# Kernel tuning notes

Measured on AMD Instinct MI355X. Metric: run time of the kernel, lower is better.

The kernel has to match this reference:

```python
import jax, jax.numpy as jnp
import numpy as np

B, S, D = 1, 2048, 4096
H, KVH, HD = 32, 8, 128
GROUPS = H // KVH  # 4
SCALE = HD ** -0.5
NEG = jnp.finfo(jnp.float32).min


def rotate_half(x):
    x1 = x[..., : x.shape[-1] // 2]
    x2 = x[..., x.shape[-1] // 2:]
    return jnp.concatenate((-x2, x1), axis=-1)


def setup_inputs() -> dict:
    key = jax.random.key(0)
    ks = jax.random.split(key, 8)
    return {
        "hidden_states": jax.random.normal(ks[0], (B, S, D), dtype=jnp.float32),
        "cos": jax.random.uniform(ks[1], (B, S, HD), dtype=jnp.float32),
        "sin": jax.random.uniform(ks[2], (B, S, HD), dtype=jnp.float32),
        "attention_mask": jnp.ones((B, S), dtype=bool),
        "wq": jax.random.normal(ks[3], (D, H * HD), dtype=jnp.float32) * 0.02,
        "wk": jax.random.normal(ks[4], (D, KVH * HD), dtype=jnp.float32) * 0.02,
        "wv": jax.random.normal(ks[5], (D, KVH * HD), dtype=jnp.float32) * 0.02,
        "wo": jax.random.normal(ks[6], (H * HD, D), dtype=jnp.float32) * 0.02,
    }


def reference(hidden_states, cos, sin, attention_mask, wq, wk, wv, wo):
    b, s, _ = hidden_states.shape
    # projections -> (B,S,heads,head_dim)
    q = (hidden_states @ wq).reshape(b, s, H, HD)
    k = (hidden_states @ wk).reshape(b, s, KVH, HD)
    v = (hidden_states @ wv).reshape(b, s, KVH, HD)
    # RoPE (cos/sin unsqueezed at head axis)
    c = cos[:, :, None, :]
    si = sin[:, :, None, :]
    q = q * c + rotate_half(q) * si
    k = k * c + rotate_half(k) * si
    # GQA: repeat kv heads (cache_index=0, max_len==S -> cache write is identity)
    k = jnp.repeat(k, GROUPS, axis=2)
    v = jnp.repeat(v, GROUPS, axis=2)
    # mask: causal AND padding; bias 0 / -inf
    causal = jnp.tril(jnp.ones((s, s), dtype=bool))[None, None]  # (1,1,S,S)
    mask = causal & attention_mask[:, None, None, :]  # (B,1,S,S)
    bias = jnp.where(mask, 0.0, NEG).astype(hidden_states.dtype)
    # scores (B,H,S,S)
    scores = jnp.einsum("bqhd,bkhd->bhqk", q, k) * SCALE + bias
    attn = jax.nn.softmax(scores, axis=-1)
    out = jnp.einsum("bhqk,bkhd->bqhd", attn, v).reshape(b, s, H * HD)
    return out @ wo
```

## Files before the change

### kernel.cpp

```cpp
#include <hip/hip_runtime.h>
#include <hip/hip_bf16.h>

#define SEQ   2048
#define DM    4096
#define NH    32
#define NKVH  8
#define HD    128
#define NQKV  6144
#define KOFF  4096
#define VOFF  5120
#define QLD   5120
#define SCALE 0.08838834764831845f

typedef __attribute__((ext_vector_type(4))) float f32x4;
typedef __attribute__((ext_vector_type(8))) short short8;

__device__ __forceinline__ unsigned short f2bf(float f) {
  union { float f; unsigned int u; } v; v.f = f;
  unsigned int r = v.u + 0x7FFF + ((v.u >> 16) & 1);
  return (unsigned short)(r >> 16);
}
__device__ __forceinline__ float bf2f(unsigned short b) {
  union { unsigned int u; float f; } v; v.u = ((unsigned int)b) << 16;
  return v.f;
}

__device__ __forceinline__ void gld16(const unsigned short* g, unsigned short* l) {
  __builtin_amdgcn_global_load_lds(
      (const __attribute__((address_space(1))) unsigned int*)g,
      (__attribute__((address_space(3))) unsigned int*)l, 16, 0, 0);
}

__global__ __launch_bounds__(256) void prep(const float* __restrict__ hs,
                                            const float* __restrict__ wq,
                                            const float* __restrict__ wk,
                                            const float* __restrict__ wv,
                                            const float* __restrict__ wo,
                                            unsigned short* __restrict__ hsb,
                                            unsigned short* __restrict__ wqkvT,
                                            unsigned short* __restrict__ woT) {
  __shared__ unsigned short t[64][68];
  const int bxg = blockIdx.x;
  const int tid = threadIdx.x;
  if (bxg < 8192) {
    size_t i = ((size_t)bxg * 256 + tid) * 4;
    float4 v = *(const float4*)(hs + i);
    ushort4 o;
    o.x = f2bf(v.x); o.y = f2bf(v.y); o.z = f2bf(v.z); o.w = f2bf(v.w);
    *(ushort4*)(hsb + i) = o;
    return;
  }
  const int b  = bxg - 8192;
  const int bx = b % 160;
  const int k0 = (b / 160) * 64;
  const float* W; unsigned short* out; int N, n0, row_off;
  if (bx < 64)      { W = wq; out = wqkvT; N = 4096; n0 = bx * 64;        row_off = 0;    }
  else if (bx < 80) { W = wk; out = wqkvT; N = 1024; n0 = (bx - 64) * 64; row_off = 4096; }
  else if (bx < 96) { W = wv; out = wqkvT; N = 1024; n0 = (bx - 80) * 64; row_off = 5120; }
  else              { W = wo; out = woT;   N = 4096; n0 = (bx - 96) * 64; row_off = 0;    }

  const int lr = tid >> 4, lc = (tid & 15) * 4;
#pragma unroll
  for (int i = 0; i < 4; ++i) {
    float4 v = *(const float4*)&W[(size_t)(k0 + lr + i * 16) * N + n0 + lc];
    ushort4 u; u.x = f2bf(v.x); u.y = f2bf(v.y); u.z = f2bf(v.z); u.w = f2bf(v.w);
    *(ushort4*)&t[lr + i * 16][lc] = u;
  }
  __syncthreads();

  const int sn = tid >> 2, sk = (tid & 3) * 4;
#pragma unroll
  for (int i = 0; i < 4; ++i) {
    int kk = sk + i * 16;
    ushort4 u;
    u.x = t[kk + 0][sn]; u.y = t[kk + 1][sn];
    u.z = t[kk + 2][sn]; u.w = t[kk + 3][sn];
    *(ushort4*)&out[(size_t)(row_off + n0 + sn) * DM + k0 + kk] = u;
  }
}

__global__ __launch_bounds__(256) void gemm_bt(const unsigned short* __restrict__ A,
                                               const unsigned short* __restrict__ Bt,
                                               void* __restrict__ C,
                                               unsigned short* __restrict__ vt,
                                               int M, int N, int K, int ldc, int c_fp32) {
  __shared__ unsigned short As[2][128 * 32];
  __shared__ unsigned short Bs[2][128 * 32];
  const int tid  = threadIdx.x;
  const int m0   = blockIdx.y * 128;
  const int n0   = blockIdx.x * 128;
  const int w    = tid >> 6;
  const int lane = tid & 63;
  const int l16  = lane & 15;
  const int quad = lane >> 4;
  const int wr   = (w >> 1) * 64;
  const int wc   = (w & 1) * 64;

  f32x4 acc[4][4];
#pragma unroll
  for (int i = 0; i < 4; ++i)
#pragma unroll
    for (int j = 0; j < 4; ++j) acc[i][j] = (f32x4){0.f, 0.f, 0.f, 0.f};

  const int sr  = lane >> 2;
  const int pb  = lane & 3;
  const int sws = (sr & 3) ^ ((sr >> 2) & 3);
  const int kb  = ((pb ^ sws) << 3);
  const unsigned short* ga0 = A  + (size_t)(m0 + w * 16 + sr) * K + kb;
  const unsigned short* ga1 = A  + (size_t)(m0 + 64 + w * 16 + sr) * K + kb;
  const unsigned short* gb0 = Bt + (size_t)(n0 + w * 16 + sr) * K + kb;
  const unsigned short* gb1 = Bt + (size_t)(n0 + 64 + w * 16 + sr) * K + kb;
  const int lofs0 = (w * 16) * 32;
  const int lofs1 = (64 + w * 16) * 32;

  const int swf  = (l16 & 3) ^ ((l16 >> 2) & 3);
  const int fcol = ((quad ^ swf) << 3);

  gld16(ga0, &As[0][lofs0]);
  gld16(ga1, &As[0][lofs1]);
  gld16(gb0, &Bs[0][lofs0]);
  gld16(gb1, &Bs[0][lofs1]);

  int p = 0;
  for (int k0 = 0; k0 < K; k0 += 32) {
    __syncthreads();
    if (k0 + 32 < K) {
      gld16(ga0 + k0 + 32, &As[p ^ 1][lofs0]);
      gld16(ga1 + k0 + 32, &As[p ^ 1][lofs1]);
      gld16(gb0 + k0 + 32, &Bs[p ^ 1][lofs0]);
      gld16(gb1 + k0 + 32, &Bs[p ^ 1][lofs1]);
    }
    short8 af[4], bfr[4];
#pragma unroll
    for (int mt = 0; mt < 4; ++mt)
      af[mt] = *(const short8*)&As[p][(wr + mt * 16 + l16) * 32 + fcol];
#pragma unroll
    for (int nt = 0; nt < 4; ++nt)
      bfr[nt] = *(const short8*)&Bs[p][(wc + nt * 16 + l16) * 32 + fcol];
#pragma unroll
    for (int mt = 0; mt < 4; ++mt)
#pragma unroll
      for (int nt = 0; nt < 4; ++nt)
        acc[mt][nt] = __builtin_amdgcn_mfma_f32_16x16x32_bf16(af[mt], bfr[nt], acc[mt][nt], 0, 0, 0);
    p ^= 1;
  }

  if (vt && n0 >= VOFF) {
#pragma unroll
    for (int mt = 0; mt < 4; ++mt)
#pragma unroll
      for (int nt = 0; nt < 4; ++nt) {
        int col  = (n0 - VOFF) + wc + nt * 16 + l16;
        int row0 = m0 + wr + mt * 16 + quad * 4;
        ushort4 ov;
        ov.x = f2bf(acc[mt][nt][0]); ov.y = f2bf(acc[mt][nt][1]);
        ov.z = f2bf(acc[mt][nt][2]); ov.w = f2bf(acc[mt][nt][3]);
        *(ushort4*)&vt[(size_t)col * SEQ + row0] = ov;
      }
  } else if (c_fp32) {
    float* Cf = (float*)C;
#pragma unroll
    for (int mt = 0; mt < 4; ++mt)
#pragma unroll
      for (int nt = 0; nt < 4; ++nt) {
        int col = n0 + wc + nt * 16 + l16;
#pragma unroll
        for (int r = 0; r < 4; ++r)
          Cf[(size_t)(m0 + wr + mt * 16 + quad * 4 + r) * ldc + col] = acc[mt][nt][r];
      }
  } else {
    unsigned short* Cb = (unsigned short*)C;
#pragma unroll
    for (int mt = 0; mt < 4; ++mt)
#pragma unroll
      for (int nt = 0; nt < 4; ++nt) {
        int col = n0 + wc + nt * 16 + l16;
#pragma unroll
        for (int r = 0; r < 4; ++r)
          Cb[(size_t)(m0 + wr + mt * 16 + quad * 4 + r) * ldc + col] = f2bf(acc[mt][nt][r]);
      }
  }
}

__global__ __launch_bounds__(256) void rope_kernel(unsigned short* __restrict__ QKV,
                                                   const float* __restrict__ cosb,
                                                   const float* __restrict__ sinb) {
  int idx = blockIdx.x * 256 + threadIdx.x;
  int i = idx & 63;
  int h = (idx >> 6) % 40;
  int s = idx / 2560;
  size_t base = (size_t)s * QLD + (size_t)h * 128;
  float q1 = bf2f(QKV[base + i]);
  float q2 = bf2f(QKV[base + i + 64]);
  float c1 = cosb[s * 128 + i],      s1 = sinb[s * 128 + i];
  float c2 = cosb[s * 128 + i + 64], s2 = sinb[s * 128 + i + 64];
  QKV[base + i]      = f2bf(q1 * c1 - q2 * s1);
  QKV[base + i + 64] = f2bf(q2 * c2 + q1 * s2);
}

__global__ __launch_bounds__(256) void flash_attn(const unsigned short* __restrict__ QKV,
                                                  const unsigned short* __restrict__ Vt_g,
                                                  unsigned short* __restrict__ AO) {
  __shared__ unsigned short Ks[64 * 136];
  __shared__ unsigned short Vs[128 * 72];
  __shared__ unsigned short Ps[4][32 * 68];

  const int h   = blockIdx.x;
  const int qt  = (int)gridDim.y - 1 - (int)blockIdx.y;
  const int kvh = h >> 2;
  const int tid  = threadIdx.x;
  const int w    = tid >> 6;
  const int lane = tid & 63;
  const int l16  = lane & 15;
  const int quad = lane >> 4;
  const int q0   = qt * 128;
  const int qrow_w = q0 + w * 32;

  short8 qf[2][4];
#pragma unroll
  for (int ntq = 0; ntq < 2; ++ntq) {
    const unsigned short* qp = QKV + (size_t)(qrow_w + ntq * 16 + l16) * QLD + h * HD + quad * 8;
#pragma unroll
    for (int ks = 0; ks < 4; ++ks) qf[ntq][ks] = *(const short8*)(qp + ks * 32);
  }

  f32x4 o[8][2];
#pragma unroll
  for (int i = 0; i < 8; ++i) { o[i][0] = (f32x4){0,0,0,0}; o[i][1] = (f32x4){0,0,0,0}; }
  float m_i[2] = {-3.0e38f, -3.0e38f}, l_i[2] = {0.f, 0.f};

  const int kr = tid >> 2, kcol0 = (tid & 3) * 32;
  const int vr = tid >> 1, vcol0 = (tid & 1) * 32;
  const unsigned short* kbase = QKV + KOFF + (size_t)kvh * HD + kcol0;
  const unsigned short* vbase = Vt_g + ((size_t)kvh * HD + vr) * SEQ + vcol0;

  const int nch = qt * 2 + 2;
  for (int c = 0; c < nch; ++c) {
    const int kc = c * 64;
    short8 kv[4], vv[4];
#pragma unroll
    for (int u = 0; u < 4; ++u) kv[u] = *(const short8*)(kbase + (size_t)(kc + kr) * QLD + u * 8);
#pragma unroll
    for (int u = 0; u < 4; ++u) vv[u] = *(const short8*)(vbase + kc + u * 8);
    __syncthreads();
#pragma unroll
    for (int u = 0; u < 4; ++u) *(short8*)&Ks[kr * 136 + kcol0 + u * 8] = kv[u];
#pragma unroll
    for (int u = 0; u < 4; ++u) *(short8*)&Vs[vr * 72 + vcol0 + u * 8] = vv[u];
    __syncthreads();

    if (kc <= qrow_w + 31) {
      f32x4 st[4][2];
#pragma unroll
      for (int mt = 0; mt < 4; ++mt) { st[mt][0] = (f32x4){0,0,0,0}; st[mt][1] = (f32x4){0,0,0,0}; }
#pragma unroll
      for (int ks = 0; ks < 4; ++ks)
#pragma unroll
        for (int mt = 0; mt < 4; ++mt) {
          short8 ak = *(const short8*)&Ks[(mt * 16 + l16) * 136 + ks * 32 + quad * 8];
          st[mt][0] = __builtin_amdgcn_mfma_f32_16x16x32_bf16(ak, qf[0][ks], st[mt][0], 0, 0, 0);
          st[mt][1] = __builtin_amdgcn_mfma_f32_16x16x32_bf16(ak, qf[1][ks], st[mt][1], 0, 0, 0);
        }

      float sc[4][2][4];
#pragma unroll
      for (int mt = 0; mt < 4; ++mt)
#pragma unroll
        for (int ntq = 0; ntq < 2; ++ntq) {
          int qr = qrow_w + ntq * 16 + l16;
#pragma unroll
          for (int r = 0; r < 4; ++r) {
            int key = kc + mt * 16 + quad * 4 + r;
            float v = st[mt][ntq][r] * SCALE;
            sc[mt][ntq][r] = (key <= qr) ? v : -__builtin_inff();
          }
        }
      float mx[2] = {-__builtin_inff(), -__builtin_inff()};
#pragma unroll
      for (int mt = 0; mt < 4; ++mt)
#pragma unroll
        for (int ntq = 0; ntq < 2; ++ntq)
#pragma unroll
          for (int r = 0; r < 4; ++r) mx[ntq] = fmaxf(mx[ntq], sc[mt][ntq][r]);
#pragma unroll
      for (int ntq = 0; ntq < 2; ++ntq) {
        mx[ntq] = fmaxf(mx[ntq], __shfl_xor(mx[ntq], 16, 64));
        mx[ntq] = fmaxf(mx[ntq], __shfl_xor(mx[ntq], 32, 64));
      }
      float al[2], mn[2];
#pragma unroll
      for (int ntq = 0; ntq < 2; ++ntq) {
        mn[ntq] = fmaxf(m_i[ntq], mx[ntq]);
        al[ntq] = __expf(m_i[ntq] - mn[ntq]);
        m_i[ntq] = mn[ntq];
      }

      float rs[2] = {0.f, 0.f};
      unsigned short* psw = &Ps[w][0];
#pragma unroll
      for (int mt = 0; mt < 4; ++mt)
#pragma unroll
        for (int ntq = 0; ntq < 2; ++ntq) {
          float p0 = __expf(sc[mt][ntq][0] - mn[ntq]);
          float p1 = __expf(sc[mt][ntq][1] - mn[ntq]);
          float p2 = __expf(sc[mt][ntq][2] - mn[ntq]);
          float p3 = __expf(sc[mt][ntq][3] - mn[ntq]);
          rs[ntq] += (p0 + p1) + (p2 + p3);
          ushort4 pk; pk.x = f2bf(p0); pk.y = f2bf(p1); pk.z = f2bf(p2); pk.w = f2bf(p3);
          *(ushort4*)&psw[(ntq * 16 + l16) * 68 + mt * 16 + quad * 4] = pk;
        }
#pragma unroll
      for (int ntq = 0; ntq < 2; ++ntq) {
        rs[ntq] += __shfl_xor(rs[ntq], 16, 64);
        rs[ntq] += __shfl_xor(rs[ntq], 32, 64);
        l_i[ntq] = l_i[ntq] * al[ntq] + rs[ntq];
      }
#pragma unroll
      for (int i = 0; i < 8; ++i) {
        o[i][0][0] *= al[0]; o[i][0][1] *= al[0]; o[i][0][2] *= al[0]; o[i][0][3] *= al[0];
        o[i][1][0] *= al[1]; o[i][1][1] *= al[1]; o[i][1][2] *= al[1]; o[i][1][3] *= al[1];
      }

#pragma unroll
      for (int ks = 0; ks < 2; ++ks) {
        short8 bp[2];
#pragma unroll
        for (int ntq = 0; ntq < 2; ++ntq) {
          union { ushort4 h[2]; short8 v; } u;
          const unsigned short* pp = &psw[(ntq * 16 + l16) * 68 + ks * 32 + quad * 8];
          u.h[0] = *(const ushort4*)(pp);
          u.h[1] = *(const ushort4*)(pp + 4);
          bp[ntq] = u.v;
        }
#pragma unroll
        for (int mt = 0; mt < 8; ++mt) {
          short8 av = *(const short8*)&Vs[(mt * 16 + l16) * 72 + ks * 32 + quad * 8];
          o[mt][0] = __builtin_amdgcn_mfma_f32_16x16x32_bf16(av, bp[0], o[mt][0], 0, 0, 0);
          o[mt][1] = __builtin_amdgcn_mfma_f32_16x16x32_bf16(av, bp[1], o[mt][1], 0, 0, 0);
        }
      }
    }
  }

  float inv[2] = {1.0f / l_i[0], 1.0f / l_i[1]};
#pragma unroll
  for (int mt = 0; mt < 8; ++mt)
#pragma unroll
    for (int ntq = 0; ntq < 2; ++ntq) {
      int qr = qrow_w + ntq * 16 + l16;
      int col = h * HD + mt * 16 + quad * 4;
      ushort4 ov;
      ov.x = f2bf(o[mt][ntq][0] * inv[ntq]);
      ov.y = f2bf(o[mt][ntq][1] * inv[ntq]);
      ov.z = f2bf(o[mt][ntq][2] * inv[ntq]);
      ov.w = f2bf(o[mt][ntq][3] * inv[ntq]);
      *(ushort4*)&AO[(size_t)qr * DM + col] = ov;
    }
}

extern "C" void kernel_launch(void* const* d_in, const int* in_sizes, int n_in,
                              void* d_out, int out_size, void* d_ws, size_t ws_size,
                              hipStream_t stream) {
  const float* hs   = (const float*)d_in[0];
  const float* cosb = (const float*)d_in[1];
  const float* sinb = (const float*)d_in[2];
  const float* wq = (const float*)d_in[4];
  const float* wk = (const float*)d_in[5];
  const float* wv = (const float*)d_in[6];
  const float* wo = (const float*)d_in[7];
  float* out = (float*)d_out;

  char* ws = (char*)d_ws;
  unsigned short* hsb   = (unsigned short*)(ws);
  unsigned short* wqkvT = (unsigned short*)(ws + (16u << 20));
  unsigned short* woT   = (unsigned short*)(ws + (64u << 20));
  unsigned short* qkv   = (unsigned short*)(ws + (96u << 20));
  unsigned short* ao    = (unsigned short*)(ws + (116u << 20));
  unsigned short* Vt_g  = (unsigned short*)(ws + (132u << 20));

  prep<<<8192 + 160 * 64, 256, 0, stream>>>(hs, wq, wk, wv, wo, hsb, wqkvT, woT);
  gemm_bt<<<dim3(NQKV / 128, SEQ / 128), 256, 0, stream>>>(hsb, wqkvT, qkv, Vt_g, SEQ, NQKV, DM, QLD, 0);
  rope_kernel<<<20480, 256, 0, stream>>>(qkv, cosb, sinb);
  flash_attn<<<dim3(NH, SEQ / 128), 256, 0, stream>>>(qkv, Vt_g, ao);
  gemm_bt<<<dim3(DM / 128, SEQ / 128), 256, 0, stream>>>(ao, woT, out, nullptr, SEQ, DM, DM, DM, 1);
}
```

Measured before the change: 536.3 us.

## Replace GEMM with 8-wave large-tile kernel with explicit vmcnt pipelining

Replaces the 4-wave 128x128 bf16 MFMA GEMM with a templated 512-thread kernel. It uses 256x256 tiles for the QKV projection and 128x256 tiles for the output projection, with a K-step of 64 and an XOR-swizzled LDS layout. It double-buffers global-to-LDS loads using explicit s_waitcnt vmcnt counts, remaps block indices so neighbouring tiles spread across chiplets, and raises wave priority around the MFMA bursts. The goal is more operand reuse per LDS load and less barrier and load-latency stall. The cost is fewer blocks for the QKV GEMM (192 on a GPU with about 256 CUs), which may leave CUs idle, and heavy LDS use per block.

```diff
diff --git a/kernel.cpp b/kernel.cpp
--- a/kernel.cpp
+++ b/kernel.cpp
@@ -79,75 +79,108 @@
   }
 }
 
-__global__ __launch_bounds__(256) void gemm_bt(const unsigned short* __restrict__ A,
-                                               const unsigned short* __restrict__ Bt,
-                                               void* __restrict__ C,
-                                               unsigned short* __restrict__ vt,
-                                               int M, int N, int K, int ldc, int c_fp32) {
-  __shared__ unsigned short As[2][128 * 32];
-  __shared__ unsigned short Bs[2][128 * 32];
-  const int tid  = threadIdx.x;
-  const int m0   = blockIdx.y * 128;
-  const int n0   = blockIdx.x * 128;
+template <int BM, int BN>
+__global__ __launch_bounds__(512, 2) void gemm8p(const unsigned short* __restrict__ A,
+                                                 const unsigned short* __restrict__ Bt,
+                                                 void* __restrict__ C,
+                                                 unsigned short* __restrict__ vt,
+                                                 int K, int ldc, int c_fp32) {
+  constexpr int MT  = BM / 32;
+  constexpr int LPT = (BM + BN) / 64;
+  __shared__ __align__(16) unsigned short As[2][BM * 64];
+  __shared__ __align__(16) unsigned short Bs[2][BN * 64];
+
+  const int tid = threadIdx.x;
+  const int nx = gridDim.x;
+  int lin = blockIdx.y * nx + blockIdx.x;
+  {
+    const int q = (nx * (int)gridDim.y) >> 3;
+    lin = (lin & 7) * q + (lin >> 3);
+  }
+  const int m0 = (lin / nx) * BM;
+  const int n0 = (lin % nx) * BN;
+
   const int w    = tid >> 6;
   const int lane = tid & 63;
   const int l16  = lane & 15;
   const int quad = lane >> 4;
-  const int wr   = (w >> 1) * 64;
-  const int wc   = (w & 1) * 64;
-
-  f32x4 acc[4][4];
-#pragma unroll
-  for (int i = 0; i < 4; ++i)
+  const int wm   = w >> 2;
+  const int wn   = w & 3;
+  const int wr   = wm * (MT * 16);
+  const int wc   = wn * 64;
+
+  f32x4 acc[MT][4];
+#pragma unroll
+  for (int i = 0; i < MT; ++i)
 #pragma unroll
     for (int j = 0; j < 4; ++j) acc[i][j] = (f32x4){0.f, 0.f, 0.f, 0.f};
 
-  const int sr  = lane >> 2;
-  const int pb  = lane & 3;
-  const int sws = (sr & 3) ^ ((sr >> 2) & 3);
-  const int kb  = ((pb ^ sws) << 3);
-  const unsigned short* ga0 = A  + (size_t)(m0 + w * 16 + sr) * K + kb;
-  const unsigned short* ga1 = A  + (size_t)(m0 + 64 + w * 16 + sr) * K + kb;
-  const unsigned short* gb0 = Bt + (size_t)(n0 + w * 16 + sr) * K + kb;
-  const unsigned short* gb1 = Bt + (size_t)(n0 + 64 + w * 16 + sr) * K + kb;
-  const int lofs0 = (w * 16) * 32;
-  const int lofs1 = (64 + w * 16) * 32;
-
-  const int swf  = (l16 & 3) ^ ((l16 >> 2) & 3);
-  const int fcol = ((quad ^ swf) << 3);
-
-  gld16(ga0, &As[0][lofs0]);
-  gld16(ga1, &As[0][lofs1]);
-  gld16(gb0, &Bs[0][lofs0]);
-  gld16(gb1, &Bs[0][lofs1]);
-
-  int p = 0;
-  for (int k0 = 0; k0 < K; k0 += 32) {
-    __syncthreads();
-    if (k0 + 32 < K) {
-      gld16(ga0 + k0 + 32, &As[p ^ 1][lofs0]);
-      gld16(ga1 + k0 + 32, &As[p ^ 1][lofs1]);
-      gld16(gb0 + k0 + 32, &Bs[p ^ 1][lofs0]);
-      gld16(gb1 + k0 + 32, &Bs[p ^ 1][lofs1]);
+  const int r8 = lane >> 3;
+  const int g  = (lane & 7) ^ r8;
+  const unsigned short* sA = A  + (size_t)(m0 + w * 8 + r8) * K + g * 8;
+  const unsigned short* sB = Bt + (size_t)(n0 + w * 8 + r8) * K + g * 8;
+
+  const int NT = K >> 6;
+
+  const int sw  = l16 & 7;
+  const int ck0 = (quad ^ sw) * 8;
+  const int ck1 = ((4 + quad) ^ sw) * 8;
+  const int arow = (wr + l16) * 64;
+  const int brow = (wc + l16) * 64;
+
+#pragma unroll
+  for (int i = 0; i < BM / 64; ++i)
+    gld16(sA + (size_t)i * 64 * K, &As[0][(i * 64 + w * 8) * 64]);
+#pragma unroll
+  for (int i = 0; i < BN / 64; ++i)
+    gld16(sB + (size_t)i * 64 * K, &Bs[0][(i * 64 + w * 8) * 64]);
+
+  for (int t = 0; t < NT; ++t) {
+    const int cur = t & 1;
+    if (t + 1 < NT) {
+      const int ko = (t + 1) * 64;
+#pragma unroll
+      for (int i = 0; i < BM / 64; ++i)
+        gld16(sA + (size_t)i * 64 * K + ko, &As[cur ^ 1][(i * 64 + w * 8) * 64]);
+#pragma unroll
+      for (int i = 0; i < BN / 64; ++i)
+        gld16(sB + (size_t)i * 64 * K + ko, &Bs[cur ^ 1][(i * 64 + w * 8) * 64]);
+      asm volatile("s_waitcnt vmcnt(%0)" :: "n"(LPT) : "memory");
+    } else {
+      asm volatile("s_waitcnt vmcnt(0)" ::: "memory");
     }
-    short8 af[4], bfr[4];
-#pragma unroll
-    for (int mt = 0; mt < 4; ++mt)
-      af[mt] = *(const short8*)&As[p][(wr + mt * 16 + l16) * 32 + fcol];
-#pragma unroll
-    for (int nt = 0; nt < 4; ++nt)
-      bfr[nt] = *(const short8*)&Bs[p][(wc + nt * 16 + l16) * 32 + fcol];
-#pragma unroll
-    for (int mt = 0; mt < 4; ++mt)
+    __builtin_amdgcn_s_barrier();
+
+#pragma unroll
+    for (int ks = 0; ks < 2; ++ks) {
+      const int ck = ks ? ck1 : ck0;
+      short8 bfrag[4];
 #pragma unroll
       for (int nt = 0; nt < 4; ++nt)
-        acc[mt][nt] = __builtin_amdgcn_mfma_f32_16x16x32_bf16(af[mt], bfr[nt], acc[mt][nt], 0, 0, 0);
-    p ^= 1;
+        bfrag[nt] = *(const short8*)&Bs[cur][brow + nt * 1024 + ck];
+#pragma unroll
+      for (int mh = 0; mh < MT / 4; ++mh) {
+        short8 afrag[4];
+#pragma unroll
+        for (int mi = 0; mi < 4; ++mi)
+          afrag[mi] = *(const short8*)&As[cur][arow + (mh * 4 + mi) * 1024 + ck];
+        __builtin_amdgcn_s_barrier();
+        __builtin_amdgcn_s_setprio(1);
+#pragma unroll
+        for (int mi = 0; mi < 4; ++mi)
+#pragma unroll
+          for (int nt = 0; nt < 4; ++nt)
+            acc[mh * 4 + mi][nt] = __builtin_amdgcn_mfma_f32_16x16x32_bf16(
+                afrag[mi], bfrag[nt], acc[mh * 4 + mi][nt], 0, 0, 0);
+        __builtin_amdgcn_s_setprio(0);
+        __builtin_amdgcn_s_barrier();
+      }
+    }
   }
 
   if (vt && n0 >= VOFF) {
 #pragma unroll
-    for (int mt = 0; mt < 4; ++mt)
+    for (int mt = 0; mt < MT; ++mt)
 #pragma unroll
       for (int nt = 0; nt < 4; ++nt) {
         int col  = (n0 - VOFF) + wc + nt * 16 + l16;
@@ -160,7 +193,7 @@
   } else if (c_fp32) {
     float* Cf = (float*)C;
 #pragma unroll
-    for (int mt = 0; mt < 4; ++mt)
+    for (int mt = 0; mt < MT; ++mt)
 #pragma unroll
       for (int nt = 0; nt < 4; ++nt) {
         int col = n0 + wc + nt * 16 + l16;
@@ -171,7 +204,7 @@
   } else {
     unsigned short* Cb = (unsigned short*)C;
 #pragma unroll
-    for (int mt = 0; mt < 4; ++mt)
+    for (int mt = 0; mt < MT; ++mt)
 #pragma unroll
       for (int nt = 0; nt < 4; ++nt) {
         int col = n0 + wc + nt * 16 + l16;
@@ -379,8 +412,10 @@
   unsigned short* Vt_g  = (unsigned short*)(ws + (132u << 20));
 
   prep<<<8192 + 160 * 64, 256, 0, stream>>>(hs, wq, wk, wv, wo, hsb, wqkvT, woT);
-  gemm_bt<<<dim3(NQKV / 128, SEQ / 128), 256, 0, stream>>>(hsb, wqkvT, qkv, Vt_g, SEQ, NQKV, DM, QLD, 0);
+  gemm8p<256, 256><<<dim3(NQKV / 256, SEQ / 256), 512, 0, stream>>>(
+      hsb, wqkvT, qkv, Vt_g, DM, QLD, 0);
   rope_kernel<<<20480, 256, 0, stream>>>(qkv, cosb, sinb);
   flash_attn<<<dim3(NH, SEQ / 128), 256, 0, stream>>>(qkv, Vt_g, ao);
-  gemm_bt<<<dim3(DM / 128, SEQ / 128), 256, 0, stream>>>(ao, woT, out, nullptr, SEQ, DM, DM, DM, 1);
-}
+  gemm8p<128, 256><<<dim3(DM / 256, SEQ / 128), 512, 0, stream>>>(
+      ao, woT, out, nullptr, DM, DM, 1);
+}
```

Result: slower. 607.0 us (+13.2%).

## Load K/V MFMA fragments directly from global memory, dropping LDS staging

Applied to the files above, without the earlier changes.

The flash attention kernel no longer stages K and V tiles in shared memory with block-wide barriers. Each wave now loads its MFMA operand fragments straight from global memory (relying on L1/L2 for reuse across the four waves). Each wave also runs its own per-wave causal chunk count instead of a shared block-level loop, and the MFMA sections get raised scheduling priority via s_setprio. This removes the barrier syncs and the LDS traffic, and lets waves with less causal work finish early. The cost is up to four times more global/cache load traffic per block, with no explicit prefetching to hide the latency.

```diff
diff --git a/kernel.cpp b/kernel.cpp
--- a/kernel.cpp
+++ b/kernel.cpp
@@ -201,8 +201,6 @@
 __global__ __launch_bounds__(256) void flash_attn(const unsigned short* __restrict__ QKV,
                                                   const unsigned short* __restrict__ Vt_g,
                                                   unsigned short* __restrict__ AO) {
-  __shared__ unsigned short Ks[64 * 136];
-  __shared__ unsigned short Vs[128 * 72];
   __shared__ unsigned short Ps[4][32 * 68];
 
   const int h   = blockIdx.x;
@@ -213,8 +211,7 @@
   const int lane = tid & 63;
   const int l16  = lane & 15;
   const int quad = lane >> 4;
-  const int q0   = qt * 128;
-  const int qrow_w = q0 + w * 32;
+  const int qrow_w = qt * 128 + w * 32;
 
   short8 qf[2][4];
 #pragma unroll
@@ -229,116 +226,105 @@
   for (int i = 0; i < 8; ++i) { o[i][0] = (f32x4){0,0,0,0}; o[i][1] = (f32x4){0,0,0,0}; }
   float m_i[2] = {-3.0e38f, -3.0e38f}, l_i[2] = {0.f, 0.f};
 
-  const int kr = tid >> 2, kcol0 = (tid & 3) * 32;
-  const int vr = tid >> 1, vcol0 = (tid & 1) * 32;
-  const unsigned short* kbase = QKV + KOFF + (size_t)kvh * HD + kcol0;
-  const unsigned short* vbase = Vt_g + ((size_t)kvh * HD + vr) * SEQ + vcol0;
-
-  const int nch = qt * 2 + 2;
+  const unsigned short* kfb = QKV + KOFF + (size_t)kvh * HD + (size_t)l16 * QLD + quad * 8;
+  const unsigned short* vfb = Vt_g + ((size_t)kvh * HD + l16) * SEQ + quad * 8;
+
+  const int nch = (qrow_w >> 6) + 1;
   for (int c = 0; c < nch; ++c) {
     const int kc = c * 64;
-    short8 kv[4], vv[4];
-#pragma unroll
-    for (int u = 0; u < 4; ++u) kv[u] = *(const short8*)(kbase + (size_t)(kc + kr) * QLD + u * 8);
-#pragma unroll
-    for (int u = 0; u < 4; ++u) vv[u] = *(const short8*)(vbase + kc + u * 8);
-    __syncthreads();
-#pragma unroll
-    for (int u = 0; u < 4; ++u) *(short8*)&Ks[kr * 136 + kcol0 + u * 8] = kv[u];
-#pragma unroll
-    for (int u = 0; u < 4; ++u) *(short8*)&Vs[vr * 72 + vcol0 + u * 8] = vv[u];
-    __syncthreads();
-
-    if (kc <= qrow_w + 31) {
-      f32x4 st[4][2];
-#pragma unroll
-      for (int mt = 0; mt < 4; ++mt) { st[mt][0] = (f32x4){0,0,0,0}; st[mt][1] = (f32x4){0,0,0,0}; }
-#pragma unroll
-      for (int ks = 0; ks < 4; ++ks)
-#pragma unroll
-        for (int mt = 0; mt < 4; ++mt) {
-          short8 ak = *(const short8*)&Ks[(mt * 16 + l16) * 136 + ks * 32 + quad * 8];
-          st[mt][0] = __builtin_amdgcn_mfma_f32_16x16x32_bf16(ak, qf[0][ks], st[mt][0], 0, 0, 0);
-          st[mt][1] = __builtin_amdgcn_mfma_f32_16x16x32_bf16(ak, qf[1][ks], st[mt][1], 0, 0, 0);
+
+    f32x4 st[4][2];
+#pragma unroll
+    for (int mt = 0; mt < 4; ++mt) { st[mt][0] = (f32x4){0,0,0,0}; st[mt][1] = (f32x4){0,0,0,0}; }
+    __builtin_amdgcn_s_setprio(1);
+#pragma unroll
+    for (int ks = 0; ks < 4; ++ks)
+#pragma unroll
+      for (int mt = 0; mt < 4; ++mt) {
+        short8 ak = *(const short8*)(kfb + (size_t)(kc + mt * 16) * QLD + ks * 32);
+        st[mt][0] = __builtin_amdgcn_mfma_f32_16x16x32_bf16(ak, qf[0][ks], st[mt][0], 0, 0, 0);
+        st[mt][1] = __builtin_amdgcn_mfma_f32_16x16x32_bf16(ak, qf[1][ks], st[mt][1], 0, 0, 0);
+      }
+    __builtin_amdgcn_s_setprio(0);
+
+    float sc[4][2][4];
+#pragma unroll
+    for (int mt = 0; mt < 4; ++mt)
+#pragma unroll
+      for (int ntq = 0; ntq < 2; ++ntq) {
+        int qr = qrow_w + ntq * 16 + l16;
+#pragma unroll
+        for (int r = 0; r < 4; ++r) {
+          int key = kc + mt * 16 + quad * 4 + r;
+          float v = st[mt][ntq][r] * SCALE;
+          sc[mt][ntq][r] = (key <= qr) ? v : -__builtin_inff();
         }
-
-      float sc[4][2][4];
-#pragma unroll
-      for (int mt = 0; mt < 4; ++mt)
-#pragma unroll
-        for (int ntq = 0; ntq < 2; ++ntq) {
-          int qr = qrow_w + ntq * 16 + l16;
-#pragma unroll
-          for (int r = 0; r < 4; ++r) {
-            int key = kc + mt * 16 + quad * 4 + r;
-            float v = st[mt][ntq][r] * SCALE;
-            sc[mt][ntq][r] = (key <= qr) ? v : -__builtin_inff();
-          }
-        }
-      float mx[2] = {-__builtin_inff(), -__builtin_inff()};
-#pragma unroll
-      for (int mt = 0; mt < 4; ++mt)
-#pragma unroll
-        for (int ntq = 0; ntq < 2; ++ntq)
-#pragma unroll
-          for (int r = 0; r < 4; ++r) mx[ntq] = fmaxf(mx[ntq], sc[mt][ntq][r]);
+      }
+    float mx[2] = {-__builtin_inff(), -__builtin_inff()};
+#pragma unroll
+    for (int mt = 0; mt < 4; ++mt)
+#pragma unroll
+      for (int ntq = 0; ntq < 2; ++ntq)
+#pragma unroll
+        for (int r = 0; r < 4; ++r) mx[ntq] = fmaxf(mx[ntq], sc[mt][ntq][r]);
+#pragma unroll
+    for (int ntq = 0; ntq < 2; ++ntq) {
+      mx[ntq] = fmaxf(mx[ntq], __shfl_xor(mx[ntq], 16, 64));
+      mx[ntq] = fmaxf(mx[ntq], __shfl_xor(mx[ntq], 32, 64));
+    }
+    float al[2], mn[2];
+#pragma unroll
+    for (int ntq = 0; ntq < 2; ++ntq) {
+      mn[ntq] = fmaxf(m_i[ntq], mx[ntq]);
+      al[ntq] = __expf(m_i[ntq] - mn[ntq]);
+      m_i[ntq] = mn[ntq];
+    }
+
+    float rs[2] = {0.f, 0.f};
+    unsigned short* psw = &Ps[w][0];
+#pragma unroll
+    for (int mt = 0; mt < 4; ++mt)
 #pragma unroll
       for (int ntq = 0; ntq < 2; ++ntq) {
-        mx[ntq] = fmaxf(mx[ntq], __shfl_xor(mx[ntq], 16, 64));
-        mx[ntq] = fmaxf(mx[ntq], __shfl_xor(mx[ntq], 32, 64));
-      }
-      float al[2], mn[2];
+        float p0 = __expf(sc[mt][ntq][0] - mn[ntq]);
+        float p1 = __expf(sc[mt][ntq][1] - mn[ntq]);
+        float p2 = __expf(sc[mt][ntq][2] - mn[ntq]);
+        float p3 = __expf(sc[mt][ntq][3] - mn[ntq]);
+        rs[ntq] += (p0 + p1) + (p2 + p3);
+        ushort4 pk; pk.x = f2bf(p0); pk.y = f2bf(p1); pk.z = f2bf(p2); pk.w = f2bf(p3);
+        *(ushort4*)&psw[(ntq * 16 + l16) * 68 + mt * 16 + quad * 4] = pk;
+      }
+#pragma unroll
+    for (int ntq = 0; ntq < 2; ++ntq) {
+      rs[ntq] += __shfl_xor(rs[ntq], 16, 64);
+      rs[ntq] += __shfl_xor(rs[ntq], 32, 64);
+      l_i[ntq] = l_i[ntq] * al[ntq] + rs[ntq];
+    }
+#pragma unroll
+    for (int i = 0; i < 8; ++i) {
+      o[i][0][0] *= al[0]; o[i][0][1] *= al[0]; o[i][0][2] *= al[0]; o[i][0][3] *= al[0];
+      o[i][1][0] *= al[1]; o[i][1][1] *= al[1]; o[i][1][2] *= al[1]; o[i][1][3] *= al[1];
+    }
+
+#pragma unroll
+    for (int ks = 0; ks < 2; ++ks) {
+      short8 bp[2];
 #pragma unroll
       for (int ntq = 0; ntq < 2; ++ntq) {
-        mn[ntq] = fmaxf(m_i[ntq], mx[ntq]);
-        al[ntq] = __expf(m_i[ntq] - mn[ntq]);
-        m_i[ntq] = mn[ntq];
-      }
-
-      float rs[2] = {0.f, 0.f};
-      unsigned short* psw = &Ps[w][0];
-#pragma unroll
-      for (int mt = 0; mt < 4; ++mt)
-#pragma unroll
-        for (int ntq = 0; ntq < 2; ++ntq) {
-          float p0 = __expf(sc[mt][ntq][0] - mn[ntq]);
-          float p1 = __expf(sc[mt][ntq][1] - mn[ntq]);
-          float p2 = __expf(sc[mt][ntq][2] - mn[ntq]);
-          float p3 = __expf(sc[mt][ntq][3] - mn[ntq]);
-          rs[ntq] += (p0 + p1) + (p2 + p3);
-          ushort4 pk; pk.x = f2bf(p0); pk.y = f2bf(p1); pk.z = f2bf(p2); pk.w = f2bf(p3);
-          *(ushort4*)&psw[(ntq * 16 + l16) * 68 + mt * 16 + quad * 4] = pk;
-        }
-#pragma unroll
-      for (int ntq = 0; ntq < 2; ++ntq) {
-        rs[ntq] += __shfl_xor(rs[ntq], 16, 64);
-        rs[ntq] += __shfl_xor(rs[ntq], 32, 64);
-        l_i[ntq] = l_i[ntq] * al[ntq] + rs[ntq];
-      }
-#pragma unroll
-      for (int i = 0; i < 8; ++i) {
-        o[i][0][0] *= al[0]; o[i][0][1] *= al[0]; o[i][0][2] *= al[0]; o[i][0][3] *= al[0];
-        o[i][1][0] *= al[1]; o[i][1][1] *= al[1]; o[i][1][2] *= al[1]; o[i][1][3] *= al[1];
-      }
-
-#pragma unroll
-      for (int ks = 0; ks < 2; ++ks) {
-        short8 bp[2];
-#pragma unroll
-        for (int ntq = 0; ntq < 2; ++ntq) {
-          union { ushort4 h[2]; short8 v; } u;
-          const unsigned short* pp = &psw[(ntq * 16 + l16) * 68 + ks * 32 + quad * 8];
-          u.h[0] = *(const ushort4*)(pp);
-          u.h[1] = *(const ushort4*)(pp + 4);
-          bp[ntq] = u.v;
-        }
-#pragma unroll
-        for (int mt = 0; mt < 8; ++mt) {
-          short8 av = *(const short8*)&Vs[(mt * 16 + l16) * 72 + ks * 32 + quad * 8];
-          o[mt][0] = __builtin_amdgcn_mfma_f32_16x16x32_bf16(av, bp[0], o[mt][0], 0, 0, 0);
-          o[mt][1] = __builtin_amdgcn_mfma_f32_16x16x32_bf16(av, bp[1], o[mt][1], 0, 0, 0);
-        }
-      }
+        union { ushort4 h[2]; short8 v; } u;
+        const unsigned short* pp = &psw[(ntq * 16 + l16) * 68 + ks * 32 + quad * 8];
+        u.h[0] = *(const ushort4*)(pp);
+        u.h[1] = *(const ushort4*)(pp + 4);
+        bp[ntq] = u.v;
+      }
+      __builtin_amdgcn_s_setprio(1);
+#pragma unroll
+      for (int mt = 0; mt < 8; ++mt) {
+        short8 av = *(const short8*)(vfb + (size_t)(mt * 16) * SEQ + kc + ks * 32);
+        o[mt][0] = __builtin_amdgcn_mfma_f32_16x16x32_bf16(av, bp[0], o[mt][0], 0, 0, 0);
+        o[mt][1] = __builtin_amdgcn_mfma_f32_16x16x32_bf16(av, bp[1], o[mt][1], 0, 0, 0);
+      }
+      __builtin_amdgcn_s_setprio(0);
     }
   }
 
```

Measured after the change: 633.9 us. 1.18x slower.
